# Kernel optimization log

Hardware: AMD Instinct MI355X
Metric: run time of the kernel (lower is better)

The kernel has to match this reference:

```python
import jax, jax.numpy as jnp
import numpy as np

N_NODES = 100000
N_EDGES = 1200000
K1, K2 = 4096, 256  # TopKPooling ratios (int ratio => absolute k in PyG)
NEG_SLOPE = 0.01    # nn.LeakyReLU default


def leaky(v):
    return jnp.where(v >= 0, v, NEG_SLOPE * v)


def gcn_conv(x, src, dst, w, W, b):
    """PyG GCNConv: x @ W, symmetric-normalized aggregation with self-loops, + bias.
    Removed edges are represented by weight 0 (identical math to edge removal)."""
    N = x.shape[0]
    x = x @ W                                            # [N, out]
    deg = jax.ops.segment_sum(w, dst, num_segments=N) + 1.0  # +1 self-loop
    dinv = jax.lax.rsqrt(deg)
    norm = dinv[src] * w * dinv[dst]                     # per-edge norm
    agg = jax.ops.segment_sum(x[src] * norm[:, None], dst, num_segments=N)
    agg = agg + x * (dinv * dinv)[:, None]               # self-loop term
    return agg + b


def topk_pool(x, src, dst, w, p, k):
    """PyG TopKPooling: score = tanh(x.p/||p||), keep top-k, scale by score,
    relabel edges; dropped edges get weight 0 (mapped to node 0 harmlessly)."""
    N = x.shape[0]
    score = jnp.tanh((x @ p) / jnp.linalg.norm(p))
    top_scores, perm = jax.lax.top_k(score, k)
    x_new = x[perm] * top_scores[:, None]
    mapping = jnp.zeros(N, jnp.int32).at[perm].set(jnp.arange(k, dtype=jnp.int32))
    kept = jnp.zeros(N, dtype=bool).at[perm].set(True)
    valid = kept[src] & kept[dst]
    return x_new, mapping[src], mapping[dst], jnp.where(valid, w, 0.0)


def setup_inputs() -> dict:
    key = jax.random.key(0)
    ks = jax.random.split(key, 12)
    pos = jax.random.normal(ks[0], (N_NODES, 3), dtype=jnp.float32)
    edge_index = jax.random.randint(ks[1], (2, N_EDGES), 0, N_NODES, dtype=jnp.int64)

    def glorot(k, shape):
        lim = np.sqrt(6.0 / (shape[0] + shape[-1]))
        return jax.random.uniform(k, shape, jnp.float32, -lim, lim)

    return {
        "pos": pos,
        "edge_index": edge_index,
        "W1": glorot(ks[2], (3, 64)),    "b1": jnp.zeros((64,), jnp.float32),
        "W2": glorot(ks[3], (64, 128)),  "b2": jnp.zeros((128,), jnp.float32),
        "W3": glorot(ks[4], (128, 256)), "b3": jnp.zeros((256,), jnp.float32),
        "p1": jax.random.normal(ks[5], (64,), jnp.float32),
        "p2": jax.random.normal(ks[6], (256,), jnp.float32),
        "fcW": glorot(ks[7], (256 * 256, 512)),
        "fcb": jnp.zeros((512,), jnp.float32),
    }


def reference(pos, edge_index, W1, b1, W2, b2, W3, b3, p1, p2, fcW, fcb):
    src, dst = edge_index[0], edge_index[1]
    w = jnp.ones(src.shape[0], dtype=pos.dtype)

    x = leaky(gcn_conv(pos, src, dst, w, W1, b1))          # [N, 64]
    x, src, dst, w = topk_pool(x, src, dst, w, p1, K1)     # [4096, 64]
    x = leaky(gcn_conv(x, src, dst, w, W2, b2))            # [4096, 128]
    x = leaky(gcn_conv(x, src, dst, w, W3, b3))            # [4096, 256]
    x, src, dst, w = topk_pool(x, src, dst, w, p2, K2)     # [256, 256]

    x = x.T.reshape(-1)                                    # transpose(0,1) + flatten
    return x @ fcW + fcb                                   # [512]
```

## Files before the change

### kernel.cpp

```cpp
#include <hip/hip_runtime.h>
#include <cstdint>
#include <cstddef>

#define NNODES 100000
#define NEDGES 1200000
#define KP1 4096
#define KP2 256
#define CAP_CAND 16384
#define CAP1 48
#define CAP2 48
#define NSAMP 2048
#define TAURANK 167
#define NXCD 8
#define DRANGE 12500

typedef unsigned long long u64;
typedef unsigned int u32;

__device__ __forceinline__ double leakyd(double v){ return v >= 0.0 ? v : 0.01*v; }

__device__ __forceinline__ u64 mono64(double d){
  u64 b = (u64)__double_as_longlong(d);
  return (b & 0x8000000000000000ull) ? ~b : (b | 0x8000000000000000ull);
}

__device__ __forceinline__ void get_edge(const int* eb, int flag, int e, int& s, int& d){
  if (flag){ s = eb[2*e]; d = eb[2*(NEDGES+e)]; }
  else     { s = eb[e];   d = eb[NEDGES+e]; }
}

__global__ void k_meta(const int* eb, const float* p1, const float* p2, int* meta, double* dscal){
  __shared__ double red[256];
  int t = threadIdx.x;
  double s1 = 0.0;
  if (t < 64){ double v = (double)p1[t]; s1 = v*v; }
  red[t] = s1; __syncthreads();
  for (int w = 128; w > 0; w >>= 1){ if (t < w) red[t] += red[t+w]; __syncthreads(); }
  if (t == 0) dscal[0] = 1.0 / sqrt(red[0]);
  __syncthreads();
  double v2 = (double)p2[t];
  red[t] = v2*v2; __syncthreads();
  for (int w = 128; w > 0; w >>= 1){ if (t < w) red[t] += red[t+w]; __syncthreads(); }
  if (t == 0){
    dscal[1] = 1.0 / sqrt(red[0]);
    int is64 = 1;
    for (int i = 1; i <= 127; i += 2) if (eb[i] != 0){ is64 = 0; break; }
    meta[0] = is64;
  }
}

__global__ __launch_bounds__(256) void k_scatter(const int* eb, const int* meta, int* cnt1, int* csrf){
  int e = (blockIdx.x >> 3)*256 + threadIdx.x;
  int x = blockIdx.x & 7;
  if (e >= NEDGES) return;
  int s, d; get_edge(eb, meta[0], e, s, d);
  if (d/DRANGE != x) return;
  int slot = atomicAdd(&cnt1[d], 1);
  if (slot < CAP1) csrf[(size_t)d*CAP1 + slot] = s;
}

__global__ void k_prep(const int* cnt1, const float* pos, double4* posw){
  int n = blockIdx.x*256 + threadIdx.x;
  if (n >= NNODES) return;
  double di = 1.0 / sqrt((double)cnt1[n] + 1.0);
  double4 v;
  v.x = (double)pos[3*n+0]*di;
  v.y = (double)pos[3*n+1]*di;
  v.z = (double)pos[3*n+2]*di;
  v.w = di;
  posw[n] = v;
}

__global__ __launch_bounds__(256) void k_score1(const int* cnt1, const int* csrf,
                         const double4* posw,
                         const float* W1, const float* b1, const float* p1,
                         double* aggsave, double* score1raw, u64* key1){
  int gid = blockIdx.x*256 + threadIdx.x;
  int n = gid >> 2;
  int l = gid & 3;
  if (n >= NNODES) return;
  int c = cnt1[n]; if (c > CAP1) c = CAP1;
  const int4* row = (const int4*)(csrf + (size_t)n*CAP1);
  int4 r0 = row[l];
  int4 r1 = row[l+4];
  int4 r2 = row[l+8];
  double t0 = 0.0, t1 = 0.0, t2 = 0.0;
  auto g = [&](int sidx, bool liv){
    double4 p = posw[liv ? sidx : n];
    double w = liv ? 1.0 : 0.0;
    t0 += w*p.x; t1 += w*p.y; t2 += w*p.z;
  };
  int j0 = l*4;
  g(r0.x, j0+0 < c); g(r0.y, j0+1 < c); g(r0.z, j0+2 < c); g(r0.w, j0+3 < c);
  int j1 = l*4 + 16;
  g(r1.x, j1+0 < c); g(r1.y, j1+1 < c); g(r1.z, j1+2 < c); g(r1.w, j1+3 < c);
  int j2 = l*4 + 32;
  g(r2.x, j2+0 < c); g(r2.y, j2+1 < c); g(r2.z, j2+2 < c); g(r2.w, j2+3 < c);
  for (int o = 1; o < 4; o <<= 1){
    t0 += __shfl_xor(t0, o, 64);
    t1 += __shfl_xor(t1, o, 64);
    t2 += __shfl_xor(t2, o, 64);
  }
  double4 pwn = posw[n];
  double di = pwn.w;
  t0 = (t0 + pwn.x)*di;
  t1 = (t1 + pwn.y)*di;
  t2 = (t2 + pwn.z)*di;
  if (l == 0){
    aggsave[3*n+0] = t0; aggsave[3*n+1] = t1; aggsave[3*n+2] = t2;
  }
  double acc = 0.0;
  #pragma unroll
  for (int f16 = 0; f16 < 16; ++f16){
    int f = l*16 + f16;
    double h = t0*(double)W1[f] + t1*(double)W1[64+f] + t2*(double)W1[128+f] + (double)b1[f];
    acc += leakyd(h) * (double)p1[f];
  }
  acc += __shfl_xor(acc, 1, 64);
  acc += __shfl_xor(acc, 2, 64);
  if (l == 0){
    score1raw[n] = acc;
    key1[n] = (mono64(acc) & ~0x1FFFFull) | (u64)(131071 - n);
  }
}

__global__ __launch_bounds__(256) void k_tau(const u64* key1, u64* tau){
  __shared__ u64 smp[NSAMP];
  int t = threadIdx.x;
  int sid = blockIdx.x*256 + t;
  for (int i = t; i < NSAMP; i += 256) smp[i] = key1[(size_t)i*48];
  __syncthreads();
  u64 mykey = smp[sid];
  int rank = 0;
  for (int j = 0; j < NSAMP; ++j) rank += (smp[j] > mykey) ? 1 : 0;
  if (rank == TAURANK) tau[0] = mykey;
}

__global__ void k_collect(const u64* key1, const u64* tau, int* cand, u64* candkey, int* cnt){
  int n = blockIdx.x*256 + threadIdx.x;
  if (n >= NNODES) return;
  u64 k = key1[n];
  if (k >= tau[0]){
    int p = atomicAdd(&cnt[0], 1);
    if (p < CAP_CAND){ cand[p] = n; candkey[p] = k; }
  }
}

__global__ __launch_bounds__(256) void k_rankA(const u64* candkey, const int* cnt, int* rank){
  int C = cnt[0]; if (C > CAP_CAND) C = CAP_CAND;
  int ci = blockIdx.x, kj = blockIdx.y;
  if (ci*256 >= C || kj*256 >= C) return;
  __shared__ u64 tile[256];
  int t = threadIdx.x;
  int kidx = kj*256 + t;
  tile[t] = (kidx < C) ? candkey[kidx] : 0ull;
  __syncthreads();
  int idx = ci*256 + t;
  if (idx >= C) return;
  u64 mykey = candkey[idx];
  int r = 0;
  #pragma unroll 8
  for (int j = 0; j < 256; ++j) r += (tile[j] > mykey) ? 1 : 0;
  if (r) atomicAdd(&rank[idx], r);
}

__global__ void k_rankB(const int* cand, const int* cnt, const int* rank,
                        int* perm1, int* mapping){
  int idx = blockIdx.x*256 + threadIdx.x;
  int C = cnt[0]; if (C > CAP_CAND) C = CAP_CAND;
  if (idx >= C) return;
  int r = rank[idx];
  if (r < KP1){
    int node = cand[idx];
    perm1[r] = node;
    mapping[node] = r;
  }
}

__global__ __launch_bounds__(256) void k_pool1(const int* perm1, const int* cnt1, const int* csrf,
                          const int* mapping, const double* aggsave, const double* score1raw,
                          const float* W1, const float* b1, const double* dscal,
                          int* csr2, int* deg2, double* dinv2, double* x1p){
  int r = blockIdx.x*4 + (threadIdx.x >> 6);
  int l = threadIdx.x & 63;
  int n = perm1[r];
  int c = cnt1[n]; if (c > CAP1) c = CAP1;
  int m = -1;
  if (l < c) m = mapping[csrf[(size_t)n*CAP1 + l]];
  u64 bal = __ballot(m >= 0);
  int pre = __popcll(bal & ((1ull << l) - 1ull));
  if (m >= 0 && pre < CAP2) csr2[r*CAP2 + pre] = m;
  if (l == 0){
    int k = __popcll(bal); if (k > CAP2) k = CAP2;
    deg2[r] = k;
    dinv2[r] = 1.0 / sqrt((double)k + 1.0);
  }
  double sc = tanh(score1raw[n] * dscal[0]);
  double t0 = aggsave[3*n+0], t1 = aggsave[3*n+1], t2 = aggsave[3*n+2];
  double h = t0*(double)W1[l] + t1*(double)W1[64+l] + t2*(double)W1[128+l] + (double)b1[l];
  x1p[r*64+l] = leakyd(h) * sc;
}

__global__ __launch_bounds__(128) void k_x2(const int* csr2, const int* deg2, const double* dinv2,
                                            const double* x1p, const float* W2, const float* b2, double* x2){
  __shared__ double xin[64];
  int r = blockIdx.x, t = threadIdx.x;
  double dr = dinv2[r];
  if (t < 64){
    double a = 0.0;
    int c = deg2[r];
    for (int j = 0; j < c; ++j){
      int s = csr2[r*CAP2+j];
      a += x1p[s*64+t]*dinv2[s];
    }
    xin[t] = a*dr + x1p[r*64+t]*dr*dr;
  }
  __syncthreads();
  double acc = 0.0;
  for (int c = 0; c < 64; ++c) acc += xin[c]*(double)W2[c*128+t];
  x2[r*128+t] = leakyd(acc + (double)b2[t]);
}

__global__ __launch_bounds__(256) void k_x3(const int* csr2, const int* deg2, const double* dinv2,
                                            const double* x2, const float* W3, const float* b3,
                                            const float* p2, const double* dscal,
                                            double* x3, double* score2, u64* key2){
  __shared__ double xin[128];
  __shared__ double red[256];
  int r = blockIdx.x, t = threadIdx.x;
  double dr = dinv2[r];
  if (t < 128){
    double a = 0.0;
    int c = deg2[r];
    for (int j = 0; j < c; ++j){
      int s = csr2[r*CAP2+j];
      a += x2[s*128+t]*dinv2[s];
    }
    xin[t] = a*dr + x2[r*128+t]*dr*dr;
  }
  __syncthreads();
  double acc = 0.0;
  for (int c = 0; c < 128; ++c) acc += xin[c]*(double)W3[c*256+t];
  double val = leakyd(acc + (double)b3[t]);
  x3[r*256+t] = val;
  red[t] = val * (double)p2[t];
  __syncthreads();
  for (int w = 128; w > 0; w >>= 1){ if (t < w) red[t] += red[t+w]; __syncthreads(); }
  if (t == 0){
    score2[r] = tanh(red[0] * dscal[1]);
    key2[r] = (mono64(red[0]) & ~0x1FFFFull) | (u64)(131071 - r);
  }
}

__global__ __launch_bounds__(256) void k_rank2A(const u64* key2, int* rank2){
  __shared__ u64 tile[256];
  int t = threadIdx.x;
  tile[t] = key2[blockIdx.y*256 + t];
  __syncthreads();
  int idx = blockIdx.x*256 + t;
  u64 mykey = key2[idx];
  int r = 0;
  #pragma unroll 8
  for (int j = 0; j < 256; ++j) r += (tile[j] > mykey) ? 1 : 0;
  if (r) atomicAdd(&rank2[idx], r);
}

__global__ void k_rank2B(const int* rank2, const double* score2, int* perm2, double* sc2){
  int idx = blockIdx.x*256 + threadIdx.x;
  int r = rank2[idx];
  if (r < KP2){
    perm2[r] = idx;
    sc2[r] = score2[idx];
  }
}

__global__ __launch_bounds__(512) void k_fc(const double* x3, const int* perm2, const double* sc2,
                                            const float* fcW, double* partial){
  __shared__ double xs[128];
  int b = blockIdx.x, t = threadIdx.x;
  if (t < 128){
    int f = b >> 1;
    int n = ((b & 1) << 7) + t;
    xs[t] = x3[(size_t)perm2[n]*256 + f] * sc2[n];
  }
  __syncthreads();
  const float* Wp = fcW + (size_t)b*128*512 + t;
  double acc = 0.0;
  #pragma unroll 8
  for (int i = 0; i < 128; ++i) acc += xs[i]*(double)Wp[(size_t)i*512];
  partial[b*512+t] = acc;
}

__global__ __launch_bounds__(128) void k_out(const double* partial, const float* fcb, float* out){
  __shared__ double red[128];
  int o = blockIdx.x, t = threadIdx.x;
  double a = 0.0;
  for (int b = t; b < 512; b += 128) a += partial[(size_t)b*512+o];
  red[t] = a; __syncthreads();
  for (int w = 64; w > 0; w >>= 1){ if (t < w) red[t] += red[t+w]; __syncthreads(); }
  if (t == 0) out[o] = (float)(red[0] + (double)fcb[o]);
}

extern "C" void kernel_launch(void* const* d_in, const int* in_sizes, int n_in,
                              void* d_out, int out_size, void* d_ws, size_t ws_size,
                              hipStream_t stream){
  const float* pos = (const float*)d_in[0];
  const int*   eb  = (const int*)d_in[1];
  const float* W1  = (const float*)d_in[2];
  const float* b1  = (const float*)d_in[3];
  const float* W2  = (const float*)d_in[4];
  const float* b2  = (const float*)d_in[5];
  const float* W3  = (const float*)d_in[6];
  const float* b3  = (const float*)d_in[7];
  const float* p1  = (const float*)d_in[8];
  const float* p2  = (const float*)d_in[9];
  const float* fcW = (const float*)d_in[10];
  const float* fcb = (const float*)d_in[11];
  float* out = (float*)d_out;

  char* w = (char*)d_ws;
  size_t off = 0;
  auto alloc = [&](size_t bytes)->char*{
    char* p = w + off; off = (off + bytes + 255) & ~(size_t)255; return p;
  };
  int*   cnt1   = (int*)  alloc((size_t)NNODES*4);
  int*   cnt    = (int*)  alloc(64*4);
  int*   rank1  = (int*)  alloc(CAP_CAND*4);
  int*   rank2  = (int*)  alloc(KP1*4);
  size_t zero_bytes = off;
  int*   mapping= (int*)  alloc((size_t)NNODES*4);
  int*    meta  = (int*)  alloc(64*4);
  double* dscal = (double*)alloc(8*8);
  u64*   tau    = (u64*)  alloc(8*8);
  double4* posw = (double4*)alloc((size_t)NNODES*32);
  double* aggsave=(double*)alloc((size_t)NNODES*3*8);
  double* score1= (double*)alloc((size_t)NNODES*8);
  u64*   key1   = (u64*)  alloc((size_t)NNODES*8);
  int*   cand   = (int*)  alloc(CAP_CAND*4);
  u64*   candkey= (u64*)  alloc(CAP_CAND*8);
  int*   perm1  = (int*)  alloc(KP1*4);
  double* x1p   = (double*)alloc((size_t)KP1*64*8);
  int*   csr2   = (int*)  alloc((size_t)KP1*CAP2*4);
  int*   deg2   = (int*)  alloc(KP1*4);
  double* dinv2 = (double*)alloc(KP1*8);
  char*  csrf_base = alloc((size_t)NNODES*CAP1*4);
  int*   csrf   = (int*)csrf_base;
  size_t aoff = 0;
  auto alloc2 = [&](size_t bytes)->char*{
    char* p = csrf_base + aoff; aoff = (aoff + bytes + 255) & ~(size_t)255; return p;
  };
  double* x2    = (double*)alloc2((size_t)KP1*128*8);
  double* x3    = (double*)alloc2((size_t)KP1*256*8);
  double* score2= (double*)alloc2(KP1*8);
  u64*   key2   = (u64*)  alloc2(KP1*8);
  int*   perm2  = (int*)  alloc2(KP2*4);
  double* sc2   = (double*)alloc2(KP2*8);
  double* partial=(double*)alloc2((size_t)512*512*8);
  if (off > ws_size) return;

  hipMemsetAsync(d_ws, 0, zero_bytes, stream);
  hipMemsetAsync(mapping, 0xFF, (size_t)NNODES*4, stream);

  k_meta<<<1,256,0,stream>>>(eb, p1, p2, meta, dscal);
  k_scatter<<<((NEDGES+255)/256)*NXCD,256,0,stream>>>(eb, meta, cnt1, csrf);
  k_prep<<<(NNODES+255)/256,256,0,stream>>>(cnt1, pos, posw);
  k_score1<<<(NNODES*4+255)/256,256,0,stream>>>(cnt1, csrf, posw, W1, b1, p1,
                                                aggsave, score1, key1);
  k_tau<<<NSAMP/256,256,0,stream>>>(key1, tau);
  k_collect<<<(NNODES+255)/256,256,0,stream>>>(key1, tau, cand, candkey, cnt);
  {
    dim3 g(CAP_CAND/256, CAP_CAND/256);
    k_rankA<<<g,256,0,stream>>>(candkey, cnt, rank1);
  }
  k_rankB<<<CAP_CAND/256,256,0,stream>>>(cand, cnt, rank1, perm1, mapping);
  k_pool1<<<KP1/4,256,0,stream>>>(perm1, cnt1, csrf, mapping, aggsave, score1, W1, b1, dscal,
                                  csr2, deg2, dinv2, x1p);
  k_x2<<<KP1,128,0,stream>>>(csr2, deg2, dinv2, x1p, W2, b2, x2);
  k_x3<<<KP1,256,0,stream>>>(csr2, deg2, dinv2, x2, W3, b3, p2, dscal, x3, score2, key2);
  {
    dim3 g(KP1/256, KP1/256);
    k_rank2A<<<g,256,0,stream>>>(key2, rank2);
  }
  k_rank2B<<<KP1/256,256,0,stream>>>(rank2, score2, perm2, sc2);
  k_fc<<<512,512,0,stream>>>(x3, perm2, sc2, fcW, partial);
  k_out<<<512,128,0,stream>>>(partial, fcb, out);
}
```

Measured before the change: 220.8 us.

## Replace capped CSR build with edge-parallel atomic aggregation and compaction

Drops the per-node capped CSR (csrf) scatter. Degrees are now counted in one edge pass and neighbour features are summed with double-precision atomics in a second edge pass. The pooled-graph CSR is built by a third edge pass over all edges using the mapping, and per-node normalisation is recomputed from deg2 inside k_x2/k_x3. This avoids writing and reading the large 100000×48 CSR buffer and removes the CAP1 truncation, but adds two extra full passes over the 1.2M edges and 3.6M float64 atomics.

```diff
diff --git a/kernel.cpp b/kernel.cpp
--- a/kernel.cpp
+++ b/kernel.cpp
@@ -7,7 +7,6 @@
 #define KP1 4096
 #define KP2 256
 #define CAP_CAND 16384
-#define CAP1 48
 #define CAP2 48
 #define NSAMP 2048
 #define TAURANK 167
@@ -24,9 +23,11 @@
   return (b & 0x8000000000000000ull) ? ~b : (b | 0x8000000000000000ull);
 }
 
-__device__ __forceinline__ void get_edge(const int* eb, int flag, int e, int& s, int& d){
-  if (flag){ s = eb[2*e]; d = eb[2*(NEDGES+e)]; }
-  else     { s = eb[e];   d = eb[NEDGES+e]; }
+__device__ __forceinline__ int get_d(const int* eb, int flag, int e){
+  return flag ? eb[2*(NEDGES+e)] : eb[NEDGES+e];
+}
+__device__ __forceinline__ int get_s(const int* eb, int flag, int e){
+  return flag ? eb[2*e] : eb[e];
 }
 
 __global__ void k_meta(const int* eb, const float* p1, const float* p2, int* meta, double* dscal){
@@ -49,20 +50,19 @@
   }
 }
 
-__global__ __launch_bounds__(256) void k_scatter(const int* eb, const int* meta, int* cnt1, int* csrf){
+__global__ __launch_bounds__(256) void k_deg(const int* eb, const int* meta, int* deg1){
   int e = (blockIdx.x >> 3)*256 + threadIdx.x;
   int x = blockIdx.x & 7;
   if (e >= NEDGES) return;
-  int s, d; get_edge(eb, meta[0], e, s, d);
+  int d = get_d(eb, meta[0], e);
   if (d/DRANGE != x) return;
-  int slot = atomicAdd(&cnt1[d], 1);
-  if (slot < CAP1) csrf[(size_t)d*CAP1 + slot] = s;
-}
-
-__global__ void k_prep(const int* cnt1, const float* pos, double4* posw){
+  atomicAdd(&deg1[d], 1);
+}
+
+__global__ void k_prep(const int* deg1, const float* pos, double4* posw){
   int n = blockIdx.x*256 + threadIdx.x;
   if (n >= NNODES) return;
-  double di = 1.0 / sqrt((double)cnt1[n] + 1.0);
+  double di = 1.0 / sqrt((double)deg1[n] + 1.0);
   double4 v;
   v.x = (double)pos[3*n+0]*di;
   v.y = (double)pos[3*n+1]*di;
@@ -71,57 +71,39 @@
   posw[n] = v;
 }
 
-__global__ __launch_bounds__(256) void k_score1(const int* cnt1, const int* csrf,
-                         const double4* posw,
+__global__ __launch_bounds__(256) void k_agg(const int* eb, const int* meta,
+                                             const double4* posw, double* agg){
+  int e = (blockIdx.x >> 3)*256 + threadIdx.x;
+  int x = blockIdx.x & 7;
+  if (e >= NEDGES) return;
+  int flag = meta[0];
+  int d = get_d(eb, flag, e);
+  if (d/DRANGE != x) return;
+  int s = get_s(eb, flag, e);
+  double4 p = posw[s];
+  atomicAdd(&agg[3*d+0], p.x);
+  atomicAdd(&agg[3*d+1], p.y);
+  atomicAdd(&agg[3*d+2], p.z);
+}
+
+__global__ __launch_bounds__(256) void k_score(const double* agg, const double4* posw,
                          const float* W1, const float* b1, const float* p1,
-                         double* aggsave, double* score1raw, u64* key1){
-  int gid = blockIdx.x*256 + threadIdx.x;
-  int n = gid >> 2;
-  int l = gid & 3;
+                         double* score1raw, u64* key1){
+  int n = blockIdx.x*256 + threadIdx.x;
   if (n >= NNODES) return;
-  int c = cnt1[n]; if (c > CAP1) c = CAP1;
-  const int4* row = (const int4*)(csrf + (size_t)n*CAP1);
-  int4 r0 = row[l];
-  int4 r1 = row[l+4];
-  int4 r2 = row[l+8];
-  double t0 = 0.0, t1 = 0.0, t2 = 0.0;
-  auto g = [&](int sidx, bool liv){
-    double4 p = posw[liv ? sidx : n];
-    double w = liv ? 1.0 : 0.0;
-    t0 += w*p.x; t1 += w*p.y; t2 += w*p.z;
-  };
-  int j0 = l*4;
-  g(r0.x, j0+0 < c); g(r0.y, j0+1 < c); g(r0.z, j0+2 < c); g(r0.w, j0+3 < c);
-  int j1 = l*4 + 16;
-  g(r1.x, j1+0 < c); g(r1.y, j1+1 < c); g(r1.z, j1+2 < c); g(r1.w, j1+3 < c);
-  int j2 = l*4 + 32;
-  g(r2.x, j2+0 < c); g(r2.y, j2+1 < c); g(r2.z, j2+2 < c); g(r2.w, j2+3 < c);
-  for (int o = 1; o < 4; o <<= 1){
-    t0 += __shfl_xor(t0, o, 64);
-    t1 += __shfl_xor(t1, o, 64);
-    t2 += __shfl_xor(t2, o, 64);
-  }
   double4 pwn = posw[n];
   double di = pwn.w;
-  t0 = (t0 + pwn.x)*di;
-  t1 = (t1 + pwn.y)*di;
-  t2 = (t2 + pwn.z)*di;
-  if (l == 0){
-    aggsave[3*n+0] = t0; aggsave[3*n+1] = t1; aggsave[3*n+2] = t2;
-  }
+  double t0 = (agg[3*n+0] + pwn.x)*di;
+  double t1 = (agg[3*n+1] + pwn.y)*di;
+  double t2 = (agg[3*n+2] + pwn.z)*di;
   double acc = 0.0;
-  #pragma unroll
-  for (int f16 = 0; f16 < 16; ++f16){
-    int f = l*16 + f16;
+  #pragma unroll 8
+  for (int f = 0; f < 64; ++f){
     double h = t0*(double)W1[f] + t1*(double)W1[64+f] + t2*(double)W1[128+f] + (double)b1[f];
     acc += leakyd(h) * (double)p1[f];
   }
-  acc += __shfl_xor(acc, 1, 64);
-  acc += __shfl_xor(acc, 2, 64);
-  if (l == 0){
-    score1raw[n] = acc;
-    key1[n] = (mono64(acc) & ~0x1FFFFull) | (u64)(131071 - n);
-  }
+  score1raw[n] = acc;
+  key1[n] = (mono64(acc) & ~0x1FFFFull) | (u64)(131071 - n);
 }
 
 __global__ __launch_bounds__(256) void k_tau(const u64* key1, u64* tau){
@@ -177,41 +159,52 @@
   }
 }
 
-__global__ __launch_bounds__(256) void k_pool1(const int* perm1, const int* cnt1, const int* csrf,
-                          const int* mapping, const double* aggsave, const double* score1raw,
+__global__ __launch_bounds__(256) void k_pool1(const int* perm1, const double* agg,
+                          const double4* posw, const double* score1raw,
                           const float* W1, const float* b1, const double* dscal,
-                          int* csr2, int* deg2, double* dinv2, double* x1p){
+                          double* x1p){
   int r = blockIdx.x*4 + (threadIdx.x >> 6);
   int l = threadIdx.x & 63;
   int n = perm1[r];
-  int c = cnt1[n]; if (c > CAP1) c = CAP1;
-  int m = -1;
-  if (l < c) m = mapping[csrf[(size_t)n*CAP1 + l]];
-  u64 bal = __ballot(m >= 0);
-  int pre = __popcll(bal & ((1ull << l) - 1ull));
-  if (m >= 0 && pre < CAP2) csr2[r*CAP2 + pre] = m;
-  if (l == 0){
-    int k = __popcll(bal); if (k > CAP2) k = CAP2;
-    deg2[r] = k;
-    dinv2[r] = 1.0 / sqrt((double)k + 1.0);
-  }
+  double4 pwn = posw[n];
+  double di = pwn.w;
+  double t0 = (agg[3*n+0] + pwn.x)*di;
+  double t1 = (agg[3*n+1] + pwn.y)*di;
+  double t2 = (agg[3*n+2] + pwn.z)*di;
   double sc = tanh(score1raw[n] * dscal[0]);
-  double t0 = aggsave[3*n+0], t1 = aggsave[3*n+1], t2 = aggsave[3*n+2];
   double h = t0*(double)W1[l] + t1*(double)W1[64+l] + t2*(double)W1[128+l] + (double)b1[l];
   x1p[r*64+l] = leakyd(h) * sc;
 }
 
-__global__ __launch_bounds__(128) void k_x2(const int* csr2, const int* deg2, const double* dinv2,
+__global__ __launch_bounds__(256) void k_compact(const int* eb, const int* meta,
+                          const int* mapping, int* deg2, int* csr2){
+  int e = (blockIdx.x >> 3)*256 + threadIdx.x;
+  int x = blockIdx.x & 7;
+  if (e >= NEDGES) return;
+  int flag = meta[0];
+  int d = get_d(eb, flag, e);
+  if (d/DRANGE != x) return;
+  int md = mapping[d];
+  if (md < 0) return;
+  int ms = mapping[get_s(eb, flag, e)];
+  if (ms < 0) return;
+  int slot = atomicAdd(&deg2[md], 1);
+  if (slot < CAP2) csr2[md*CAP2 + slot] = ms;
+}
+
+__global__ __launch_bounds__(128) void k_x2(const int* csr2, const int* deg2,
                                             const double* x1p, const float* W2, const float* b2, double* x2){
   __shared__ double xin[64];
   int r = blockIdx.x, t = threadIdx.x;
-  double dr = dinv2[r];
+  int cr = deg2[r]; if (cr > CAP2) cr = CAP2;
+  double dr = 1.0 / sqrt((double)cr + 1.0);
   if (t < 64){
     double a = 0.0;
-    int c = deg2[r];
-    for (int j = 0; j < c; ++j){
+    for (int j = 0; j < cr; ++j){
       int s = csr2[r*CAP2+j];
-      a += x1p[s*64+t]*dinv2[s];
+      int cs = deg2[s]; if (cs > CAP2) cs = CAP2;
+      double ds = 1.0 / sqrt((double)cs + 1.0);
+      a += x1p[s*64+t]*ds;
     }
     xin[t] = a*dr + x1p[r*64+t]*dr*dr;
   }
@@ -221,20 +214,22 @@
   x2[r*128+t] = leakyd(acc + (double)b2[t]);
 }
 
-__global__ __launch_bounds__(256) void k_x3(const int* csr2, const int* deg2, const double* dinv2,
+__global__ __launch_bounds__(256) void k_x3(const int* csr2, const int* deg2,
                                             const double* x2, const float* W3, const float* b3,
                                             const float* p2, const double* dscal,
                                             double* x3, double* score2, u64* key2){
   __shared__ double xin[128];
   __shared__ double red[256];
   int r = blockIdx.x, t = threadIdx.x;
-  double dr = dinv2[r];
+  int cr = deg2[r]; if (cr > CAP2) cr = CAP2;
+  double dr = 1.0 / sqrt((double)cr + 1.0);
   if (t < 128){
     double a = 0.0;
-    int c = deg2[r];
-    for (int j = 0; j < c; ++j){
+    for (int j = 0; j < cr; ++j){
       int s = csr2[r*CAP2+j];
-      a += x2[s*128+t]*dinv2[s];
+      int cs = deg2[s]; if (cs > CAP2) cs = CAP2;
+      double ds = 1.0 / sqrt((double)cs + 1.0);
+      a += x2[s*128+t]*ds;
     }
     xin[t] = a*dr + x2[r*128+t]*dr*dr;
   }
@@ -323,7 +318,9 @@
   auto alloc = [&](size_t bytes)->char*{
     char* p = w + off; off = (off + bytes + 255) & ~(size_t)255; return p;
   };
-  int*   cnt1   = (int*)  alloc((size_t)NNODES*4);
+  int*   deg1   = (int*)  alloc((size_t)NNODES*4);
+  double* agg   = (double*)alloc((size_t)NNODES*3*8);
+  int*   deg2   = (int*)  alloc(KP1*4);
   int*   cnt    = (int*)  alloc(64*4);
   int*   rank1  = (int*)  alloc(CAP_CAND*4);
   int*   rank2  = (int*)  alloc(KP1*4);
@@ -333,7 +330,6 @@
   double* dscal = (double*)alloc(8*8);
   u64*   tau    = (u64*)  alloc(8*8);
   double4* posw = (double4*)alloc((size_t)NNODES*32);
-  double* aggsave=(double*)alloc((size_t)NNODES*3*8);
   double* score1= (double*)alloc((size_t)NNODES*8);
   u64*   key1   = (u64*)  alloc((size_t)NNODES*8);
   int*   cand   = (int*)  alloc(CAP_CAND*4);
@@ -341,31 +337,24 @@
   int*   perm1  = (int*)  alloc(KP1*4);
   double* x1p   = (double*)alloc((size_t)KP1*64*8);
   int*   csr2   = (int*)  alloc((size_t)KP1*CAP2*4);
-  int*   deg2   = (int*)  alloc(KP1*4);
-  double* dinv2 = (double*)alloc(KP1*8);
-  char*  csrf_base = alloc((size_t)NNODES*CAP1*4);
-  int*   csrf   = (int*)csrf_base;
-  size_t aoff = 0;
-  auto alloc2 = [&](size_t bytes)->char*{
-    char* p = csrf_base + aoff; aoff = (aoff + bytes + 255) & ~(size_t)255; return p;
-  };
-  double* x2    = (double*)alloc2((size_t)KP1*128*8);
-  double* x3    = (double*)alloc2((size_t)KP1*256*8);
-  double* score2= (double*)alloc2(KP1*8);
-  u64*   key2   = (u64*)  alloc2(KP1*8);
-  int*   perm2  = (int*)  alloc2(KP2*4);
-  double* sc2   = (double*)alloc2(KP2*8);
-  double* partial=(double*)alloc2((size_t)512*512*8);
+  double* x2    = (double*)alloc((size_t)KP1*128*8);
+  double* x3    = (double*)alloc((size_t)KP1*256*8);
+  double* score2= (double*)alloc(KP1*8);
+  u64*   key2   = (u64*)  alloc(KP1*8);
+  int*   perm2  = (int*)  alloc(KP2*4);
+  double* sc2   = (double*)alloc(KP2*8);
+  double* partial=(double*)alloc((size_t)512*512*8);
   if (off > ws_size) return;
 
   hipMemsetAsync(d_ws, 0, zero_bytes, stream);
   hipMemsetAsync(mapping, 0xFF, (size_t)NNODES*4, stream);
 
+  int eblocks = ((NEDGES+255)/256)*NXCD;
   k_meta<<<1,256,0,stream>>>(eb, p1, p2, meta, dscal);
-  k_scatter<<<((NEDGES+255)/256)*NXCD,256,0,stream>>>(eb, meta, cnt1, csrf);
-  k_prep<<<(NNODES+255)/256,256,0,stream>>>(cnt1, pos, posw);
-  k_score1<<<(NNODES*4+255)/256,256,0,stream>>>(cnt1, csrf, posw, W1, b1, p1,
-                                                aggsave, score1, key1);
+  k_deg<<<eblocks,256,0,stream>>>(eb, meta, deg1);
+  k_prep<<<(NNODES+255)/256,256,0,stream>>>(deg1, pos, posw);
+  k_agg<<<eblocks,256,0,stream>>>(eb, meta, posw, agg);
+  k_score<<<(NNODES+255)/256,256,0,stream>>>(agg, posw, W1, b1, p1, score1, key1);
   k_tau<<<NSAMP/256,256,0,stream>>>(key1, tau);
   k_collect<<<(NNODES+255)/256,256,0,stream>>>(key1, tau, cand, candkey, cnt);
   {
@@ -373,10 +362,10 @@
     k_rankA<<<g,256,0,stream>>>(candkey, cnt, rank1);
   }
   k_rankB<<<CAP_CAND/256,256,0,stream>>>(cand, cnt, rank1, perm1, mapping);
-  k_pool1<<<KP1/4,256,0,stream>>>(perm1, cnt1, csrf, mapping, aggsave, score1, W1, b1, dscal,
-                                  csr2, deg2, dinv2, x1p);
-  k_x2<<<KP1,128,0,stream>>>(csr2, deg2, dinv2, x1p, W2, b2, x2);
-  k_x3<<<KP1,256,0,stream>>>(csr2, deg2, dinv2, x2, W3, b3, p2, dscal, x3, score2, key2);
+  k_pool1<<<KP1/4,256,0,stream>>>(perm1, agg, posw, score1, W1, b1, dscal, x1p);
+  k_compact<<<eblocks,256,0,stream>>>(eb, meta, mapping, deg2, csr2);
+  k_x2<<<KP1,128,0,stream>>>(csr2, deg2, x1p, W2, b2, x2);
+  k_x3<<<KP1,256,0,stream>>>(csr2, deg2, x2, W3, b3, p2, dscal, x3, score2, key2);
   {
     dim3 g(KP1/256, KP1/256);
     k_rank2A<<<g,256,0,stream>>>(key2, rank2);
```

Result: slower. 385.5 us (+74.6%).
